# Performance work log

Measured on AMD Instinct MI355X. Metric: run time of the kernel, lower is better.

Reference implementation:

```python
import jax, jax.numpy as jnp
import numpy as np

K = 20
EPS = 1e-5
SLOPE = 0.2

def _bn(x, g, b, ch_axis=1):
    # eval-mode BatchNorm: running_mean=0, running_var=1
    shape = [1] * x.ndim
    shape[ch_axis] = -1
    scale = (g / jnp.sqrt(1.0 + EPS)).reshape(shape)
    return x * scale + b.reshape(shape)

def _knn_idx(x, k):
    # x: [B, C, N] -> idx [B, N, k] of nearest neighbors in feature space (self included)
    xx = jnp.sum(x * x, axis=1)                      # [B, N]
    inner = jnp.einsum('bcn,bcm->bnm', x, x)         # [B, N, N]
    d2 = xx[:, :, None] - 2.0 * inner + xx[:, None, :]
    _, idx = jax.lax.top_k(-d2, k)
    return idx

def _edge_conv(x, w, g, b, k=K):
    # x: [B, C, N]; w: [O, 2C]
    idx = _knn_idx(x, k)                              # [B, N, k]
    nb = jax.vmap(lambda f, i: f[:, i])(x, idx)       # [B, C, N, k]
    center = x[:, :, :, None]                         # [B, C, N, 1]
    e = jnp.concatenate([nb - center, jnp.broadcast_to(center, nb.shape)], axis=1)  # [B, 2C, N, k]
    y = jnp.einsum('oc,bcnk->bonk', w, e)
    y = jax.nn.leaky_relu(_bn(y, g, b), SLOPE)
    return jnp.max(y, axis=3)                         # [B, O, N]

def setup_inputs() -> dict:
    key = jax.random.key(0)
    ks = iter(jax.random.split(key, 32))
    def w(shape, s=0.05):
        return jax.random.normal(next(ks), shape, dtype=jnp.float32) * s
    def gm(n):
        return 1.0 + 0.1 * jax.random.normal(next(ks), (n,), dtype=jnp.float32)
    def bt(n):
        return 0.1 * jax.random.normal(next(ks), (n,), dtype=jnp.float32)
    B, N, NC = 8, 2048, 40
    inp = {
        'points': jax.random.normal(next(ks), (B, 3, N), dtype=jnp.float32),
        'ec1_w': w((64, 6)),   'ec1_g': gm(64),  'ec1_b': bt(64),
        'ec2_w': w((64, 128)), 'ec2_g': gm(64),  'ec2_b': bt(64),
        'ec3_w': w((128, 128)),'ec3_g': gm(128), 'ec3_b': bt(128),
        'ec4_w': w((256, 256)),'ec4_g': gm(256), 'ec4_b': bt(256),
        'mlp_w': w((1024, 512)),'mlp_g': gm(1024),'mlp_b': bt(1024),
        'fc1_w': w((512, 2048)),'fc1_bias': bt(512),'fc1_g': gm(512),'fc1_b': bt(512),
        'fc2_w': w((256, 512)), 'fc2_bias': bt(256),'fc2_g': gm(256),'fc2_b': bt(256),
        'fc3_w': w((NC, 256)),  'fc3_bias': bt(NC),
    }
    return inp

def reference(points, ec1_w, ec1_g, ec1_b, ec2_w, ec2_g, ec2_b,
              ec3_w, ec3_g, ec3_b, ec4_w, ec4_g, ec4_b,
              mlp_w, mlp_g, mlp_b,
              fc1_w, fc1_bias, fc1_g, fc1_b,
              fc2_w, fc2_bias, fc2_g, fc2_b,
              fc3_w, fc3_bias):
    p1 = _edge_conv(points, ec1_w, ec1_g, ec1_b)      # [B, 64, N]
    p2 = _edge_conv(p1, ec2_w, ec2_g, ec2_b)          # [B, 64, N]
    p3 = _edge_conv(p2, ec3_w, ec3_g, ec3_b)          # [B, 128, N]
    p4 = _edge_conv(p3, ec4_w, ec4_g, ec4_b)          # [B, 256, N]
    x = jnp.concatenate([p1, p2, p3, p4], axis=1)     # [B, 512, N]
    x = jnp.einsum('oc,bcn->bon', mlp_w, x)           # conv1d k=1, no bias
    x = jax.nn.leaky_relu(_bn(x, mlp_g, mlp_b), SLOPE)  # [B, 1024, N]
    feat = jnp.concatenate([jnp.max(x, axis=2), jnp.mean(x, axis=2)], axis=1)  # [B, 2048]
    h = feat @ fc1_w.T + fc1_bias
    h = jax.nn.leaky_relu(_bn(h, fc1_g, fc1_b), SLOPE)  # dropout = identity (eval)
    h = h @ fc2_w.T + fc2_bias
    h = jax.nn.leaky_relu(_bn(h, fc2_g, fc2_b), SLOPE)
    return h @ fc3_w.T + fc3_bias                     # [B, num_class]
```

## Files before the change

kernel.cpp:

```cpp
#include <hip/hip_runtime.h>

#define NPTS 2048
#define BATCH 8
#define KNN 20
#define KSPLIT 4

typedef short short8v __attribute__((ext_vector_type(8)));
typedef float f32x4 __attribute__((ext_vector_type(4)));

__device__ __forceinline__ float leaky(float y) { return fmaxf(y, 0.2f * y); }

__device__ __forceinline__ short f2bf(float f) {
  unsigned u = __float_as_uint(f);
  unsigned r = (u + 0x7fffu + ((u >> 16) & 1u)) >> 16;
  return (short)r;
}
__device__ __forceinline__ float bf2f(short h) {
  return __uint_as_float(((unsigned)(unsigned short)h) << 16);
}

__device__ __forceinline__ unsigned med3u(unsigned key, unsigned lo, unsigned hi) {
  unsigned t;
  asm("v_med3_u32 %0, %1, %2, %3" : "=v"(t) : "v"(key), "v"(lo), "v"(hi));
  return t;
}

__global__ void prep_wpq_kernel(const float* __restrict__ W, const float* __restrict__ g,
                                short* __restrict__ wph, short* __restrict__ wpl,
                                int O, int C, int P2, int NCHUNK) {
  int t = blockIdx.x * 256 + threadIdx.x;
  if (t >= NCHUNK * 4 * P2) return;
  int cg = t / P2, p = t - cg * P2;
  int chunk = cg >> 2, gg = cg & 3;
  int po = (p < O) ? p : p - O;
  float s = g[po] * rsqrtf(1.0f + 1e-5f);
  short8v h8, l8;
  #pragma unroll
  for (int j = 0; j < 8; ++j) {
    int c = chunk * 32 + gg * 4 + (j & 3) + 16 * (j >> 2);
    float v = 0.f;
    if (c < C) {
      v = (p < O) ? s * W[p * 2 * C + c]
                  : s * (W[po * 2 * C + C + c] - W[po * 2 * C + c]);
    }
    short h = f2bf(v);
    h8[j] = h;
    l8[j] = f2bf(v - bf2f(h));
  }
  *reinterpret_cast<short8v*>(wph + (long)t * 8) = h8;
  *reinterpret_cast<short8v*>(wpl + (long)t * 8) = l8;
}

__global__ void prep_wq_kernel(const float* __restrict__ W, const float* __restrict__ g,
                               short* __restrict__ wqh, short* __restrict__ wql) {
  int t = blockIdx.x * 256 + threadIdx.x;
  if (t >= 64 * 1024) return;
  int cg = t >> 10, o = t & 1023;
  int chunk = cg >> 2, gg = cg & 3;
  float scale = g[o] * rsqrtf(1.0f + 1e-5f);
  short8v h8, l8;
  #pragma unroll
  for (int j = 0; j < 8; ++j) {
    int c = chunk * 32 + gg * 4 + (j & 3) + 16 * (j >> 2);
    float v = scale * W[o * 512 + c];
    short h = f2bf(v);
    h8[j] = h;
    l8[j] = f2bf(v - bf2f(h));
  }
  *reinterpret_cast<short8v*>(wqh + (long)t * 8) = h8;
  *reinterpret_cast<short8v*>(wql + (long)t * 8) = l8;
}

__global__ void xx_kernel(const float* __restrict__ x, float* __restrict__ xx,
                          int C, long bstride) {
  int b = blockIdx.y;
  int m = blockIdx.x * 256 + threadIdx.x;
  const float* xb = x + (long)b * bstride;
  float s = 0.f;
  for (int c = 0; c < C; ++c) { float v = xb[c * NPTS + m]; s += v * v; }
  xx[b * NPTS + m] = s;
}

__global__ void split_kernel(const float* __restrict__ x, short* __restrict__ xfh,
                             short* __restrict__ xfl, int C, int NCHUNK, long bstride) {
  int b = blockIdx.y;
  int t = blockIdx.x * 256 + threadIdx.x;
  int cg = t >> 11, n = t & 2047;
  int chunk = cg >> 2, g = cg & 3;
  const float* xb = x + (long)b * bstride;
  short8v h8, l8;
  #pragma unroll
  for (int j = 0; j < 8; ++j) {
    int c = chunk * 32 + g * 4 + (j & 3) + 16 * (j >> 2);
    float v = (c < C) ? xb[c * NPTS + n] : 0.f;
    short h = f2bf(v);
    float lo = v - bf2f(h);
    h8[j] = h;
    l8[j] = f2bf(lo);
  }
  long q = (long)b * NCHUNK * 4 * 2048 + t;
  *reinterpret_cast<short8v*>(xfh + q * 8) = h8;
  *reinterpret_cast<short8v*>(xfl + q * 8) = l8;
}

__global__ void mlp_split_kernel(const float* __restrict__ xcat, short* __restrict__ xqh,
                                 short* __restrict__ xql) {
  int b = blockIdx.y;
  int t = blockIdx.x * 256 + threadIdx.x;
  int cg = t >> 11, n = t & 2047;
  int chunk = cg >> 2, g = cg & 3;
  const float* xb = xcat + (long)b * 512 * NPTS;
  short8v h8, l8;
  #pragma unroll
  for (int j = 0; j < 8; ++j) {
    int c = chunk * 32 + g * 4 + (j & 3) + 16 * (j >> 2);
    float v = xb[c * NPTS + n];
    short h = f2bf(v);
    h8[j] = h;
    l8[j] = f2bf(v - bf2f(h));
  }
  long q = (long)b * 64 * 2048 + t;
  *reinterpret_cast<short8v*>(xqh + q * 8) = h8;
  *reinterpret_cast<short8v*>(xql + q * 8) = l8;
}

template <int NCHUNK>
__global__ __launch_bounds__(256, 4) void knn_scan(const short* __restrict__ xfh,
                                                   const short* __restrict__ xfl,
                                                   const float* __restrict__ xx,
                                                   unsigned* __restrict__ pd) {
  __shared__ __align__(16) float smem[2080];
  short8v* qsm = (short8v*)smem;
  unsigned* mD = (unsigned*)smem;

  int tid = threadIdx.x;
  int lane = tid & 63, wv = tid >> 6;
  int pt = lane & 15;
  int kg = lane >> 4;
  int b = blockIdx.z;
  int sidx = blockIdx.y;
  int n0 = blockIdx.x * 64;
  const float* xxb = xx + b * NPTS;
  const short8v* xfh_b = (const short8v*)xfh + (long)b * NCHUNK * 4 * 2048;
  const short8v* xfl_b = (const short8v*)xfl + (long)b * NCHUNK * 4 * 2048;

  short8v bfh[NCHUNK], bfl[NCHUNK];
  #pragma unroll
  for (int c = 0; c < NCHUNK; ++c) {
    long qi = ((long)(c * 4 + kg)) * 2048 + n0 + wv * 16 + pt;
    bfh[c] = xfh_b[qi];
    bfl[c] = xfl_b[qi];
  }
  float xn = xxb[n0 + wv * 16 + pt];

  unsigned pl[20];
  #pragma unroll
  for (int k = 0; k < 20; ++k) pl[k] = 0xFFFFFFFFu;

  int mt0 = sidx * (32 / KSPLIT);

  short8v pA, pB;
  {
    long qi = ((long)(0 * 4 + wv)) * 2048 + mt0 * 64 + lane;
    pA = xfh_b[qi];
    pB = xfl_b[qi];
  }

  for (int mtl = 0; mtl < 32 / KSPLIT; ++mtl) {
    int m0 = (mt0 + mtl) * 64;
    float xpm[4][4];
    #pragma unroll
    for (int f = 0; f < 4; ++f) {
      f32x4 q = *reinterpret_cast<const f32x4*>(&xxb[m0 + f * 16 + kg * 4]);
      #pragma unroll
      for (int r = 0; r < 4; ++r) xpm[f][r] = (xn + 4.0f) + q[r];
    }
    f32x4 acc[4];
    #pragma unroll
    for (int f = 0; f < 4; ++f) acc[f] = (f32x4){0.f, 0.f, 0.f, 0.f};

    #pragma unroll
    for (int c = 0; c < NCHUNK; ++c) {
      __syncthreads();
      qsm[wv * 65 + lane] = pA;
      qsm[(4 + wv) * 65 + lane] = pB;
      __syncthreads();
      int nm = mtl, nc = c + 1;
      if (nc == NCHUNK) { nc = 0; nm = mtl + 1; }
      if (nm < 32 / KSPLIT) {
        long qi = ((long)(nc * 4 + wv)) * 2048 + (mt0 + nm) * 64 + lane;
        pA = xfh_b[qi];
        pB = xfl_b[qi];
      }
      #pragma unroll
      for (int f = 0; f < 4; ++f) {
        short8v ah = qsm[kg * 65 + f * 16 + pt];
        short8v al = qsm[(4 + kg) * 65 + f * 16 + pt];
        acc[f] = __builtin_amdgcn_mfma_f32_16x16x32_bf16(ah, bfh[c], acc[f], 0, 0, 0);
        acc[f] = __builtin_amdgcn_mfma_f32_16x16x32_bf16(ah, bfl[c], acc[f], 0, 0, 0);
        acc[f] = __builtin_amdgcn_mfma_f32_16x16x32_bf16(al, bfh[c], acc[f], 0, 0, 0);
      }
    }

    #pragma unroll
    for (int f = 0; f < 4; ++f) {
      #pragma unroll
      for (int r = 0; r < 4; ++r) {
        float v = fmaf(-2.f, acc[f][r], xpm[f][r]);
        unsigned key = (__float_as_uint(v) & 0xFFFFF800u) | (unsigned)(m0 + f * 16 + kg * 4 + r);
        #pragma unroll
        for (int k = 19; k >= 1; --k)
          pl[k] = med3u(key, pl[k - 1], pl[k]);
        pl[0] = min(key, pl[0]);
      }
    }
  }
  __syncthreads();

  unsigned h = pl[0];
  #pragma unroll
  for (int k = 0; k < KNN; ++k) {
    unsigned v0 = (unsigned)__shfl((int)h, pt);
    unsigned v1 = (unsigned)__shfl((int)h, pt + 16);
    unsigned v2 = (unsigned)__shfl((int)h, pt + 32);
    unsigned v3 = (unsigned)__shfl((int)h, pt + 48);
    unsigned bv = v0; int bp = 0;
    if (v1 < bv) { bv = v1; bp = 1; }
    if (v2 < bv) { bv = v2; bp = 2; }
    if (v3 < bv) { bv = v3; bp = 3; }
    if (kg == 0) mD[(wv * 16 + pt) * KNN + k] = bv;
    bool pop = (kg == bp);
    #pragma unroll
    for (int i = 0; i < 19; ++i) pl[i] = pop ? pl[i + 1] : pl[i];
    pl[19] = pop ? 0xFFFFFFFFu : pl[19];
    h = pl[0];
  }
  __syncthreads();

  long base = ((long)((b * KSPLIT + sidx) * NPTS) + n0) * KNN;
  #pragma unroll
  for (int s = 0; s < 5; ++s) pd[base + s * 256 + tid] = mD[s * 256 + tid];
}

template <int NCHUNK>
__global__ __launch_bounds__(256) void vsus_mfma_kernel(const short* __restrict__ xfh,
                                                        const short* __restrict__ xfl,
                                                        const short* __restrict__ wph,
                                                        const short* __restrict__ wpl,
                                                        float* __restrict__ out, int P2) {
  __shared__ __align__(16) short8v qsmX[2 * 4 * 130];
  int tid = threadIdx.x;
  int lane = tid & 63, wv = tid >> 6;
  int pt = lane & 15, kg = lane >> 4;
  int b = blockIdx.z, pb = blockIdx.y, nt = blockIdx.x;
  int n0 = nt * 128;
  int pw = pb * 128 + (wv >> 1) * 64;
  int nwoff = (wv & 1) * 64;
  const short8v* xh_b = (const short8v*)xfh + (long)b * NCHUNK * 4 * 2048;
  const short8v* xl_b = (const short8v*)xfl + (long)b * NCHUNK * 4 * 2048;
  const short8v* wh_q = (const short8v*)wph;
  const short8v* wl_q = (const short8v*)wpl;

  f32x4 acc[4][4];
  #pragma unroll
  for (int f2 = 0; f2 < 4; ++f2)
    #pragma unroll
    for (int fb = 0; fb < 4; ++fb) acc[f2][fb] = (f32x4){0.f, 0.f, 0.f, 0.f};

  for (int chunk = 0; chunk < NCHUNK; ++chunk) {
    __syncthreads();
    #pragma unroll
    for (int s = 0; s < 4; ++s) {
      int idx = s * 256 + tid;
      int hl = idx >> 9, rem = idx & 511, g = rem >> 7, n = rem & 127;
      const short8v* src = hl ? xl_b : xh_b;
      qsmX[hl * 520 + g * 130 + n] = src[(long)(chunk * 4 + g) * 2048 + n0 + n];
    }
    __syncthreads();
    short8v ah[4], al[4];
    #pragma unroll
    for (int f2 = 0; f2 < 4; ++f2) {
      long qi = (long)(chunk * 4 + kg) * P2 + pw + f2 * 16 + pt;
      ah[f2] = wh_q[qi];
      al[f2] = wl_q[qi];
    }
    #pragma unroll
    for (int fb = 0; fb < 4; ++fb) {
      short8v bh = qsmX[0 * 520 + kg * 130 + nwoff + fb * 16 + pt];
      short8v bl = qsmX[1 * 520 + kg * 130 + nwoff + fb * 16 + pt];
      #pragma unroll
      for (int f2 = 0; f2 < 4; ++f2) {
        acc[f2][fb] = __builtin_amdgcn_mfma_f32_16x16x32_bf16(ah[f2], bh, acc[f2][fb], 0, 0, 0);
        acc[f2][fb] = __builtin_amdgcn_mfma_f32_16x16x32_bf16(al[f2], bh, acc[f2][fb], 0, 0, 0);
        acc[f2][fb] = __builtin_amdgcn_mfma_f32_16x16x32_bf16(ah[f2], bl, acc[f2][fb], 0, 0, 0);
      }
    }
  }

  #pragma unroll
  for (int f2 = 0; f2 < 4; ++f2) {
    #pragma unroll
    for (int fb = 0; fb < 4; ++fb) {
      int n = n0 + nwoff + fb * 16 + pt;
      *reinterpret_cast<f32x4*>(out + (long)(b * NPTS + n) * P2 + pw + f2 * 16 + kg * 4) =
          acc[f2][fb];
    }
  }
}

__global__ __launch_bounds__(256) void gather_max_kernel(const float* __restrict__ vsus,
                                                         const unsigned* __restrict__ pd,
                                                         const float* __restrict__ bias,
                                                         float* __restrict__ xcat,
                                                         int O, int cho) {
  __shared__ __align__(16) float smemA[640 + 256 * 33];
  int* idxs = (int*)smemA;
  unsigned* plists = (unsigned*)(smemA + 640);
  float* ot = smemA + 640;

  int tid = threadIdx.x;
  int b = blockIdx.y;
  int n0 = blockIdx.x * 32;
  int P2 = 2 * O;

  for (int i = tid; i < KSPLIT * 32 * KNN; i += 256) {
    int s = i / (32 * KNN), rem = i - s * (32 * KNN);
    plists[i] = pd[((long)((b * KSPLIT + s) * NPTS) + n0) * KNN + rem];
  }
  __syncthreads();
  if (tid < 32) {
    int h0 = 0, h1 = 0, h2 = 0, h3 = 0;
    int base = tid * KNN;
    for (int k = 0; k < KNN; ++k) {
      unsigned v0 = plists[0 * 640 + base + h0];
      unsigned v1 = plists[1 * 640 + base + h1];
      unsigned v2 = plists[2 * 640 + base + h2];
      unsigned v3 = plists[3 * 640 + base + h3];
      unsigned bv = v0; int bp = 0;
      if (v1 < bv) { bv = v1; bp = 1; }
      if (v2 < bv) { bv = v2; bp = 2; }
      if (v3 < bv) { bv = v3; bp = 3; }
      idxs[base + k] = (int)(bv & 0x7FFu);
      h0 += (bp == 0); h1 += (bp == 1); h2 += (bp == 2); h3 += (bp == 3);
    }
  }
  __syncthreads();

  int G = 256 / O;
  int o = tid % O;
  int ns = tid / O;
  float bo = bias[o];
  const float* vb = vsus + (long)b * NPTS * P2;
  for (int step = 0; step < 32 / G; ++step) {
    int nn = step * G + ns;
    float mx = -1e30f;
    for (int k = 0; k < KNN; ++k) {
      int j = idxs[nn * KNN + k];
      mx = fmaxf(mx, vb[j * P2 + o]);
    }
    float us = vb[(n0 + nn) * P2 + O + o] + bo;
    ot[o * 33 + nn] = leaky(mx + us);
  }
  __syncthreads();
  float* ob = xcat + ((long)b * 512 + cho) * NPTS + n0;
  for (int i = tid; i < O * 32; i += 256) {
    int oo = i >> 5, nn = i & 31;
    ob[oo * NPTS + nn] = ot[oo * 33 + nn];
  }
}

__global__ __launch_bounds__(256) void mlp_kernel(const short* __restrict__ xqh,
                                                  const short* __restrict__ xql,
                                                  const short* __restrict__ wqh,
                                                  const short* __restrict__ wql,
                                                  const float* __restrict__ bvec,
                                                  float* __restrict__ pbuf) {
  __shared__ __align__(16) short8v qsmX[2 * 4 * 130];
  __shared__ float redM[4][64];
  __shared__ float redS[4][64];
  int tid = threadIdx.x;
  int lane = tid & 63, wv = tid >> 6;
  int pt = lane & 15, kg = lane >> 4;
  int b = blockIdx.z, ob = blockIdx.y, nt = blockIdx.x;
  int o0 = ob * 128, n0 = nt * 128;
  int ow = o0 + (wv >> 1) * 64;
  int nwoff = (wv & 1) * 64;
  const short8v* xqh_b = (const short8v*)xqh + (long)b * 64 * 2048;
  const short8v* xql_b = (const short8v*)xql + (long)b * 64 * 2048;
  const short8v* wqh_q = (const short8v*)wqh;
  const short8v* wql_q = (const short8v*)wql;

  f32x4 acc[4][4];
  #pragma unroll
  for (int f2 = 0; f2 < 4; ++f2)
    #pragma unroll
    for (int fb = 0; fb < 4; ++fb) acc[f2][fb] = (f32x4){0.f, 0.f, 0.f, 0.f};

  for (int chunk = 0; chunk < 16; ++chunk) {
    __syncthreads();
    #pragma unroll
    for (int s = 0; s < 4; ++s) {
      int idx = s * 256 + tid;
      int hl = idx >> 9, rem = idx & 511, g = rem >> 7, n = rem & 127;
      const short8v* src = hl ? xql_b : xqh_b;
      qsmX[hl * 520 + g * 130 + n] = src[(long)(chunk * 4 + g) * 2048 + n0 + n];
    }
    __syncthreads();
    short8v ah[4], al[4];
    #pragma unroll
    for (int f2 = 0; f2 < 4; ++f2) {
      long qi = (long)(chunk * 4 + kg) * 1024 + ow + f2 * 16 + pt;
      ah[f2] = wqh_q[qi];
      al[f2] = wql_q[qi];
    }
    #pragma unroll
    for (int fb = 0; fb < 4; ++fb) {
      short8v bh = qsmX[0 * 520 + kg * 130 + nwoff + fb * 16 + pt];
      short8v bl = qsmX[1 * 520 + kg * 130 + nwoff + fb * 16 + pt];
      #pragma unroll
      for (int f2 = 0; f2 < 4; ++f2) {
        acc[f2][fb] = __builtin_amdgcn_mfma_f32_16x16x32_bf16(ah[f2], bh, acc[f2][fb], 0, 0, 0);
        acc[f2][fb] = __builtin_amdgcn_mfma_f32_16x16x32_bf16(al[f2], bh, acc[f2][fb], 0, 0, 0);
        acc[f2][fb] = __builtin_amdgcn_mfma_f32_16x16x32_bf16(ah[f2], bl, acc[f2][fb], 0, 0, 0);
      }
    }
  }

  #pragma unroll
  for (int f2 = 0; f2 < 4; ++f2) {
    #pragma unroll
    for (int r = 0; r < 4; ++r) {
      float bb = bvec[ow + f2 * 16 + kg * 4 + r];
      float mx = -1e30f, sm = 0.f;
      #pragma unroll
      for (int fb = 0; fb < 4; ++fb) {
        float y = leaky(acc[f2][fb][r] + bb);
        mx = fmaxf(mx, y);
        sm += y;
      }
      #pragma unroll
      for (int off = 1; off < 16; off <<= 1) {
        mx = fmaxf(mx, __shfl_xor(mx, off));
        sm += __shfl_xor(sm, off);
      }
      if (pt == 0) {
        redM[wv][f2 * 16 + kg * 4 + r] = mx;
        redS[wv][f2 * 16 + kg * 4 + r] = sm;
      }
    }
  }
  __syncthreads();
  if (tid < 128) {
    int os = tid >> 6, ol = tid & 63;
    float mx = fmaxf(redM[os * 2 + 0][ol], redM[os * 2 + 1][ol]);
    float sm = redS[os * 2 + 0][ol] + redS[os * 2 + 1][ol];
    float* pb = pbuf + (((long)(b * 8 + ob) * 16 + nt) * 2) * 128;
    pb[os * 64 + ol] = mx;
    pb[128 + os * 64 + ol] = sm;
  }
}

__global__ void mlp_reduce_kernel(const float* __restrict__ pbuf, float* __restrict__ feat) {
  int t = blockIdx.x * 256 + threadIdx.x;
  int b = t >> 10, o = t & 1023;
  int ob = o >> 7, ol = o & 127;
  float mx = -1e30f, s = 0.f;
  for (int nt = 0; nt < 16; ++nt) {
    const float* pb = pbuf + (((long)(b * 8 + ob) * 16 + nt) * 2) * 128;
    mx = fmaxf(mx, pb[ol]);
    s += pb[128 + ol];
  }
  feat[b * 2048 + o] = mx;
  feat[b * 2048 + 1024 + o] = s * (1.f / 2048.f);
}

__global__ void fc_kernel(const float* __restrict__ X, const float* __restrict__ W,
                          const float* __restrict__ bias, const float* __restrict__ g,
                          const float* __restrict__ bb, float* __restrict__ out,
                          int B, int O, int Kdim, int hasAct) {
  int gt = blockIdx.x * 256 + threadIdx.x;
  int wid = gt >> 6;
  int lane = threadIdx.x & 63;
  if (wid >= B * O) return;
  int b = wid / O, o = wid - b * O;
  const float* xr = X + (long)b * Kdim;
  const float* wr = W + (long)o * Kdim;
  float acc = 0.f;
  for (int c = lane; c < Kdim; c += 64) acc += xr[c] * wr[c];
  for (int off = 32; off; off >>= 1) acc += __shfl_down(acc, off);
  if (lane == 0) {
    float h = acc + bias[o];
    if (hasAct) {
      float a = g[o] * rsqrtf(1.0f + 1e-5f);
      h = a * h + bb[o];
      h = fmaxf(h, 0.2f * h);
    }
    out[b * O + o] = h;
  }
}

extern "C" void kernel_launch(void* const* d_in, const int* in_sizes, int n_in,
                              void* d_out, int out_size, void* d_ws, size_t ws_size,
                              hipStream_t stream) {
  const float* points = (const float*)d_in[0];
  char* ws = (char*)d_ws;

  const size_t XCAT = 0;
  const size_t VSUS = 33554432;
  const size_t XF   = 67108864;
  const size_t IDXB = 75497472;
  const size_t XXB  = 76808192;
  const size_t WPQ  = 76873728;
  const size_t WMLP = 77135872;
  const size_t FEAT = 79233024;
  const size_t H1   = 79298560;
  const size_t H2   = 79314944;
  const size_t KNND = 79331328;

  float* xcat = (float*)(ws + XCAT);
  float* vsus = (float*)(ws + VSUS);
  float* xxb  = (float*)(ws + XXB);
  float* feat = (float*)(ws + FEAT);
  float* h1   = (float*)(ws + H1);
  float* h2   = (float*)(ws + H2);

  unsigned* knnD = (unsigned*)(ws + KNND);
  short* xfh = (short*)(ws + XF);
  short* xfl = (short*)(ws + XF + 4194304);
  short* xqh = (short*)(ws + VSUS);
  short* xql = (short*)(ws + VSUS + 16777216);
  float* pbuf = (float*)(ws + IDXB);
  short* wpqh = (short*)(ws + WPQ);
  short* wpql = (short*)(ws + WPQ + 131072);
  short* wqh = (short*)(ws + WMLP);
  short* wql = (short*)(ws + WMLP + 1048576);

  struct Layer { const float* x; long bstride; int C, O, cho, wi, gi, bi; };
  Layer layers[4] = {
    { points,              (long)3 * NPTS,   3,   64, 0,   1, 2, 3 },
    { xcat,                (long)512 * NPTS, 64,  64, 64,  4, 5, 6 },
    { xcat + 64 * NPTS,    (long)512 * NPTS, 64,  128, 128, 7, 8, 9 },
    { xcat + 128 * NPTS,   (long)512 * NPTS, 128, 256, 256, 10, 11, 12 },
  };

  for (int L = 0; L < 4; ++L) {
    Layer& ly = layers[L];
    int P2 = 2 * ly.O;
    const float* W = (const float*)d_in[ly.wi];
    const float* g = (const float*)d_in[ly.gi];
    const float* bv = (const float*)d_in[ly.bi];
    int NCHUNK = (ly.C + 31) / 32;

    prep_wpq_kernel<<<(NCHUNK * 4 * P2 + 255) / 256, 256, 0, stream>>>(
        W, g, wpqh, wpql, ly.O, ly.C, P2, NCHUNK);
    xx_kernel<<<dim3(NPTS / 256, BATCH), 256, 0, stream>>>(ly.x, xxb, ly.C, ly.bstride);
    split_kernel<<<dim3(NCHUNK * 32, BATCH), 256, 0, stream>>>(
        ly.x, xfh, xfl, ly.C, NCHUNK, ly.bstride);
    dim3 sg(NPTS / 64, KSPLIT, BATCH);
    dim3 vg(NPTS / 128, P2 / 128, BATCH);
    if (NCHUNK == 1) {
      knn_scan<1><<<sg, 256, 0, stream>>>(xfh, xfl, xxb, knnD);
      vsus_mfma_kernel<1><<<vg, 256, 0, stream>>>(xfh, xfl, wpqh, wpql, vsus, P2);
    } else if (NCHUNK == 2) {
      knn_scan<2><<<sg, 256, 0, stream>>>(xfh, xfl, xxb, knnD);
      vsus_mfma_kernel<2><<<vg, 256, 0, stream>>>(xfh, xfl, wpqh, wpql, vsus, P2);
    } else {
      knn_scan<4><<<sg, 256, 0, stream>>>(xfh, xfl, xxb, knnD);
      vsus_mfma_kernel<4><<<vg, 256, 0, stream>>>(xfh, xfl, wpqh, wpql, vsus, P2);
    }
    gather_max_kernel<<<dim3(NPTS / 32, BATCH), 256, 0, stream>>>(
        vsus, knnD, bv, xcat, ly.O, ly.cho);
  }

  prep_wq_kernel<<<256, 256, 0, stream>>>(
      (const float*)d_in[13], (const float*)d_in[14], wqh, wql);
  mlp_split_kernel<<<dim3(512, BATCH), 256, 0, stream>>>(xcat, xqh, xql);
  mlp_kernel<<<dim3(16, 8, BATCH), 256, 0, stream>>>(
      xqh, xql, wqh, wql, (const float*)d_in[15], pbuf);
  mlp_reduce_kernel<<<32, 256, 0, stream>>>(pbuf, feat);

  fc_kernel<<<(BATCH * 512 * 64) / 256, 256, 0, stream>>>(
      feat, (const float*)d_in[16], (const float*)d_in[17],
      (const float*)d_in[18], (const float*)d_in[19], h1, BATCH, 512, 2048, 1);
  fc_kernel<<<(BATCH * 256 * 64) / 256, 256, 0, stream>>>(
      h1, (const float*)d_in[20], (const float*)d_in[21],
      (const float*)d_in[22], (const float*)d_in[23], h2, BATCH, 256, 512, 1);
  fc_kernel<<<(BATCH * 40 * 64) / 256, 256, 0, stream>>>(
      h2, (const float*)d_in[24], (const float*)d_in[25],
      nullptr, nullptr, (float*)d_out, BATCH, 40, 256, 0);
}
```

Before: 446.5 us.

## Double KNN scan split and halve MLP output tile to raise block count

Measured after the change: 467.5 us. 1.05x slower.

```diff
diff --git a/kernel.cpp b/kernel.cpp
--- a/kernel.cpp
+++ b/kernel.cpp
@@ -3,7 +3,7 @@
 #define NPTS 2048
 #define BATCH 8
 #define KNN 20
-#define KSPLIT 4
+#define KSPLIT 8
 
 typedef short short8v __attribute__((ext_vector_type(8)));
 typedef float f32x4 __attribute__((ext_vector_type(4)));
@@ -329,19 +329,20 @@
   }
   __syncthreads();
   if (tid < 32) {
-    int h0 = 0, h1 = 0, h2 = 0, h3 = 0;
+    int h[KSPLIT];
+    #pragma unroll
+    for (int s = 0; s < KSPLIT; ++s) h[s] = 0;
     int base = tid * KNN;
     for (int k = 0; k < KNN; ++k) {
-      unsigned v0 = plists[0 * 640 + base + h0];
-      unsigned v1 = plists[1 * 640 + base + h1];
-      unsigned v2 = plists[2 * 640 + base + h2];
-      unsigned v3 = plists[3 * 640 + base + h3];
-      unsigned bv = v0; int bp = 0;
-      if (v1 < bv) { bv = v1; bp = 1; }
-      if (v2 < bv) { bv = v2; bp = 2; }
-      if (v3 < bv) { bv = v3; bp = 3; }
+      unsigned bv = 0xFFFFFFFFu; int bp = 0;
+      #pragma unroll
+      for (int s = 0; s < KSPLIT; ++s) {
+        unsigned v = plists[s * 640 + base + h[s]];
+        if (v < bv) { bv = v; bp = s; }
+      }
       idxs[base + k] = (int)(bv & 0x7FFu);
-      h0 += (bp == 0); h1 += (bp == 1); h2 += (bp == 2); h3 += (bp == 3);
+      #pragma unroll
+      for (int s = 0; s < KSPLIT; ++s) h[s] += (bp == s);
     }
   }
   __syncthreads();
@@ -382,19 +383,18 @@
   int lane = tid & 63, wv = tid >> 6;
   int pt = lane & 15, kg = lane >> 4;
   int b = blockIdx.z, ob = blockIdx.y, nt = blockIdx.x;
-  int o0 = ob * 128, n0 = nt * 128;
-  int ow = o0 + (wv >> 1) * 64;
-  int nwoff = (wv & 1) * 64;
+  int ow = ob * 64, n0 = nt * 128;
+  int nwoff = wv * 32;
   const short8v* xqh_b = (const short8v*)xqh + (long)b * 64 * 2048;
   const short8v* xql_b = (const short8v*)xql + (long)b * 64 * 2048;
   const short8v* wqh_q = (const short8v*)wqh;
   const short8v* wql_q = (const short8v*)wql;
 
-  f32x4 acc[4][4];
+  f32x4 acc[4][2];
   #pragma unroll
   for (int f2 = 0; f2 < 4; ++f2)
     #pragma unroll
-    for (int fb = 0; fb < 4; ++fb) acc[f2][fb] = (f32x4){0.f, 0.f, 0.f, 0.f};
+    for (int fb = 0; fb < 2; ++fb) acc[f2][fb] = (f32x4){0.f, 0.f, 0.f, 0.f};
 
   for (int chunk = 0; chunk < 16; ++chunk) {
     __syncthreads();
@@ -414,7 +414,7 @@
       al[f2] = wql_q[qi];
     }
     #pragma unroll
-    for (int fb = 0; fb < 4; ++fb) {
+    for (int fb = 0; fb < 2; ++fb) {
       short8v bh = qsmX[0 * 520 + kg * 130 + nwoff + fb * 16 + pt];
       short8v bl = qsmX[1 * 520 + kg * 130 + nwoff + fb * 16 + pt];
       #pragma unroll
@@ -433,7 +433,7 @@
       float bb = bvec[ow + f2 * 16 + kg * 4 + r];
       float mx = -1e30f, sm = 0.f;
       #pragma unroll
-      for (int fb = 0; fb < 4; ++fb) {
+      for (int fb = 0; fb < 2; ++fb) {
         float y = leaky(acc[f2][fb][r] + bb);
         mx = fmaxf(mx, y);
         sm += y;
@@ -450,25 +450,24 @@
     }
   }
   __syncthreads();
-  if (tid < 128) {
-    int os = tid >> 6, ol = tid & 63;
-    float mx = fmaxf(redM[os * 2 + 0][ol], redM[os * 2 + 1][ol]);
-    float sm = redS[os * 2 + 0][ol] + redS[os * 2 + 1][ol];
-    float* pb = pbuf + (((long)(b * 8 + ob) * 16 + nt) * 2) * 128;
-    pb[os * 64 + ol] = mx;
-    pb[128 + os * 64 + ol] = sm;
+  if (tid < 64) {
+    float mx = fmaxf(fmaxf(redM[0][tid], redM[1][tid]), fmaxf(redM[2][tid], redM[3][tid]));
+    float sm = redS[0][tid] + redS[1][tid] + redS[2][tid] + redS[3][tid];
+    float* pb = pbuf + ((long)((b * 16 + ob) * 16 + nt)) * 128;
+    pb[tid] = mx;
+    pb[64 + tid] = sm;
   }
 }
 
 __global__ void mlp_reduce_kernel(const float* __restrict__ pbuf, float* __restrict__ feat) {
   int t = blockIdx.x * 256 + threadIdx.x;
   int b = t >> 10, o = t & 1023;
-  int ob = o >> 7, ol = o & 127;
+  int ob = o >> 6, ol = o & 63;
   float mx = -1e30f, s = 0.f;
   for (int nt = 0; nt < 16; ++nt) {
-    const float* pb = pbuf + (((long)(b * 8 + ob) * 16 + nt) * 2) * 128;
+    const float* pb = pbuf + ((long)((b * 16 + ob) * 16 + nt)) * 128;
     mx = fmaxf(mx, pb[ol]);
-    s += pb[128 + ol];
+    s += pb[64 + ol];
   }
   feat[b * 2048 + o] = mx;
   feat[b * 2048 + 1024 + o] = s * (1.f / 2048.f);
@@ -575,7 +574,7 @@
   prep_wq_kernel<<<256, 256, 0, stream>>>(
       (const float*)d_in[13], (const float*)d_in[14], wqh, wql);
   mlp_split_kernel<<<dim3(512, BATCH), 256, 0, stream>>>(xcat, xqh, xql);
-  mlp_kernel<<<dim3(16, 8, BATCH), 256, 0, stream>>>(
+  mlp_kernel<<<dim3(16, 16, BATCH), 256, 0, stream>>>(
       xqh, xql, wqh, wql, (const float*)d_in[15], pbuf);
   mlp_reduce_kernel<<<32, 256, 0, stream>>>(pbuf, feat);
 
```
